# Kernel tuning notes

Measured on AMD Instinct MI355X. Metric: run time of the kernel, lower is better.

Reference implementation:

```python
import jax, jax.numpy as jnp
import numpy as np

DIM = 2048
N_HEADS = 16
HEAD_DIM = DIM // N_HEADS

def setup_inputs() -> dict:
    key = jax.random.key(0)
    kx, kqkv, kout = jax.random.split(key, 3)
    x = jax.random.normal(kx, (2, 2048, DIM), dtype=jnp.float32)
    # nn.Linear weights stored [out_features, in_features]; y = x @ W.T
    W_qkv = jax.random.normal(kqkv, (3 * DIM, DIM), dtype=jnp.float32) * (DIM ** -0.5)
    W_out = jax.random.normal(kout, (DIM, DIM), dtype=jnp.float32) * (DIM ** -0.5)
    return {"x": x, "W_qkv": W_qkv, "W_out": W_out}

def reference(x, W_qkv, W_out):
    B, T, D = x.shape
    qkv = jnp.einsum('btd,ed->bte', x, W_qkv)  # [B,T,3D]
    q, k, v = jnp.split(qkv, 3, axis=-1)
    def heads(t):
        return t.reshape(B, T, N_HEADS, HEAD_DIM).transpose(0, 2, 1, 3)  # [B,H,T,d]
    q, k, v = heads(q), heads(k), heads(v)
    att = jnp.einsum('bhid,bhjd->bhij', q, k) / (HEAD_DIM ** 0.5)
    causal = jnp.tril(jnp.ones((T, T), dtype=bool))
    att = jnp.where(causal, att, -jnp.inf)
    att = jax.nn.softmax(att, axis=-1)
    out = jnp.einsum('bhij,bhjd->bhid', att, v)
    out = out.transpose(0, 2, 1, 3).reshape(B, T, D)
    return jnp.einsum('btd,ed->bte', out, W_out)
```

## Files before the change

### kernel.cpp

```cpp
#include <hip/hip_runtime.h>

typedef short short8 __attribute__((ext_vector_type(8)));
typedef short short4v __attribute__((ext_vector_type(4)));
typedef float f32x4 __attribute__((ext_vector_type(4)));
typedef unsigned short u16;
typedef u16 ushort4v __attribute__((ext_vector_type(4)));

__device__ inline u16 f2bf(float f){
  unsigned int u = __builtin_bit_cast(unsigned int, f);
  u = (u + 0x7fffu + ((u >> 16) & 1u)) >> 16;
  return (u16)u;
}

__device__ inline short8 cat8(short4v a, short4v b){
  short8 r;
  r[0]=a[0]; r[1]=a[1]; r[2]=a[2]; r[3]=a[3];
  r[4]=b[0]; r[5]=b[1]; r[6]=b[2]; r[7]=b[3];
  return r;
}

__device__ inline void gload_lds16(const void* g, unsigned lds_addr){
  __builtin_amdgcn_global_load_lds((__attribute__((address_space(1))) void*)(uintptr_t)g,
                                   (__attribute__((address_space(3))) void*)(uintptr_t)lds_addr,
                                   16, 0, 0);
}

__global__ void cvt_bf16(const float* __restrict__ in, u16* __restrict__ out, int n4){
  int stride = gridDim.x * blockDim.x;
  for (int i = blockIdx.x * blockDim.x + threadIdx.x; i < n4; i += stride){
    float4 v = ((const float4*)in)[i];
    ushort4v r = { f2bf(v.x), f2bf(v.y), f2bf(v.z), f2bf(v.w) };
    ((ushort4v*)out)[i] = r;
  }
}

#define BARRIER() { __builtin_amdgcn_sched_barrier(0); __builtin_amdgcn_s_barrier(); __builtin_amdgcn_sched_barrier(0); }
#define VM4() asm volatile("s_waitcnt vmcnt(4)" ::: "memory");

#define MFMA4(MO, AA, BB) { __builtin_amdgcn_s_setprio(1); \
  _Pragma("unroll") for (int m = 0; m < 4; m++) \
    _Pragma("unroll") for (int n = 0; n < 4; n++) \
      acc[(MO)+m][n] = __builtin_amdgcn_mfma_f32_16x16x32_bf16(AA[(MO)+m], BB[n], acc[(MO)+m][n], 0, 0, 0); \
  __builtin_amdgcn_s_setprio(0); }

#define PHASE4(ABASE, BBASE, ST1, ST2, ST3, ST4) { \
    const u16* Ab = (ABASE); const u16* Bb = (BBASE); \
    short8 a0[8], b0[4], a1[8], b1[4]; \
    _Pragma("unroll") for (int m = 0; m < 8; m++){ int row = wm*128 + m*16 + lr; int ph = lg ^ (row & 7); a0[m] = *(const short8*)&Ab[row*64 + ph*8]; } \
    _Pragma("unroll") for (int n = 0; n < 4; n++){ int row = wn*64 + n*16 + lr; int ph = lg ^ (row & 7); b0[n] = *(const short8*)&Bb[row*64 + ph*8]; } \
    ST1 BARRIER() MFMA4(0, a0, b0) BARRIER() \
    _Pragma("unroll") for (int m = 0; m < 8; m++){ int row = wm*128 + m*16 + lr; int ph = (4+lg) ^ (row & 7); a1[m] = *(const short8*)&Ab[row*64 + ph*8]; } \
    _Pragma("unroll") for (int n = 0; n < 4; n++){ int row = wn*64 + n*16 + lr; int ph = (4+lg) ^ (row & 7); b1[n] = *(const short8*)&Bb[row*64 + ph*8]; } \
    ST2 BARRIER() MFMA4(4, a0, b0) BARRIER() \
    ST3 BARRIER() MFMA4(0, a1, b1) BARRIER() \
    ST4 VM4() BARRIER() MFMA4(4, a1, b1) BARRIER() \
  }

template<int OUT_BF16>
__global__ __launch_bounds__(512, 2) void gemm256(const u16* __restrict__ A, const u16* __restrict__ B,
                                                  void* __restrict__ Cv, int M, int N, int K){
  __shared__ u16 lds[2][32768];
  const int tid = threadIdx.x, wave = tid >> 6, lane = tid & 63;
  const int lr = lane & 15, lg = lane >> 4;
  const int wm = wave >> 2, wn = wave & 3;
  const long bm = blockIdx.x * 256L, bn = blockIdx.y * 256L;
  const int l3 = lane >> 3, l7 = lane & 7;

  const u16* asrc = A + (bm + wave*8 + l3) * (long)K + (l7 ^ l3) * 8;
  const u16* bsrc = B + (bn + wave*8 + l3) * (long)K + (l7 ^ l3) * 8;
  const unsigned ldsbase = (unsigned)(uintptr_t)&lds[0][0];
  const unsigned wdst = wave * 1024u;

#define STG_A(BUF,S,KOFF) gload_lds16(asrc + (size_t)(S)*64*K + (KOFF), ldsbase + (BUF)*65536u + wdst + (S)*8192u);
#define STG_B(BUF,S,KOFF) gload_lds16(bsrc + (size_t)(S)*64*K + (KOFF), ldsbase + (BUF)*65536u + 32768u + wdst + (S)*8192u);

  f32x4 acc[8][4] = {};
  const int nk = K >> 6;

  #pragma unroll
  for (int s = 0; s < 4; s++){ STG_A(0, s, 0) }
  #pragma unroll
  for (int s = 0; s < 4; s++){ STG_B(0, s, 0) }
  #pragma unroll
  for (int s = 0; s < 4; s++){ STG_A(1, s, 64) }
  VM4()
  BARRIER()

  for (int i = 0; i < (nk >> 1); i++){
    const size_t kt1 = (size_t)((2*i + 1) << 6);
    const size_t kn0 = (size_t)(((2*i + 2) & (nk - 1)) << 6);
    const size_t kn1 = (size_t)(((2*i + 3) & (nk - 1)) << 6);
    PHASE4(&lds[0][0], &lds[0][16384],
           STG_B(1,0,kt1) STG_B(1,1,kt1),
           STG_B(1,2,kt1) STG_B(1,3,kt1),
           STG_A(0,0,kn0) STG_A(0,1,kn0),
           STG_A(0,2,kn0) STG_A(0,3,kn0))
    PHASE4(&lds[1][0], &lds[1][16384],
           STG_B(0,0,kn0) STG_B(0,1,kn0),
           STG_B(0,2,kn0) STG_B(0,3,kn0),
           STG_A(1,0,kn1) STG_A(1,1,kn1),
           STG_A(1,2,kn1) STG_A(1,3,kn1))
  }
#undef STG_A
#undef STG_B

  #pragma unroll
  for (int m = 0; m < 8; m++){
    #pragma unroll
    for (int n = 0; n < 4; n++){
      #pragma unroll
      for (int r = 0; r < 4; r++){
        long row = bm + wm*128 + m*16 + lg*4 + r;
        long col = bn + wn*64 + n*16 + lr;
        float v = acc[m][n][r];
        if (OUT_BF16) ((u16*)Cv)[row * (long)N + col] = f2bf(v);
        else          ((float*)Cv)[row * (long)N + col] = v;
      }
    }
  }
}

template<int OUT_BF16>
__global__ __launch_bounds__(512, 2) void gemm_bt2(const u16* __restrict__ A, const u16* __restrict__ B,
                                                   void* __restrict__ Cv, int M, int N, int K){
  __shared__ u16 lds[2][24576];
  const int tid = threadIdx.x, wave = tid >> 6, lane = tid & 63;
  const int lr = lane & 15, lg = lane >> 4;
  const int wm = wave >> 2, wn = wave & 3;
  const long bm = blockIdx.x * 128L, bn = blockIdx.y * 256L;
  const int l3 = lane >> 3, l7 = lane & 7;

  const u16* asrc = A + (bm + wave * 8 + l3) * (long)K + (l7 ^ l3) * 8;
  const u16* bsrc = B + (bn + wave * 8 + l3) * (long)K + (l7 ^ l3) * 8;
  const unsigned ldsbase = (unsigned)(uintptr_t)&lds[0][0];
  const unsigned adst = wave * 1024u;
  const unsigned bdst = 16384u + wave * 1024u;

  #define STAGE(BUF, K0) { \
    unsigned bb = ldsbase + (unsigned)(BUF) * 49152u; \
    gload_lds16(asrc + (K0),                       bb + adst); \
    gload_lds16(asrc + 64 * (size_t)K + (K0),      bb + adst + 8192u); \
    gload_lds16(bsrc + (K0),                       bb + bdst); \
    gload_lds16(bsrc + 64 * (size_t)K + (K0),      bb + bdst + 8192u); \
    gload_lds16(bsrc + 128 * (size_t)K + (K0),     bb + bdst + 16384u); \
    gload_lds16(bsrc + 192 * (size_t)K + (K0),     bb + bdst + 24576u); \
  }

  f32x4 acc[4][4] = {};
  const int nk = K >> 6;
  int cur = 0;

  STAGE(0, 0)
  asm volatile("s_waitcnt vmcnt(0)" ::: "memory");
  BARRIER()

  for (int t = 0; t < nk; ++t){
    if (t + 1 < nk){
      STAGE(cur ^ 1, (t + 1) * 64)
      asm volatile("s_waitcnt vmcnt(6)" ::: "memory");
    } else {
      asm volatile("s_waitcnt vmcnt(0)" ::: "memory");
    }
    BARRIER()

    const u16* Ab = &lds[cur][0];
    const u16* Bb = &lds[cur][8192];
    short8 af[2][4], bfr[2][4];
    #pragma unroll
    for (int kk = 0; kk < 2; kk++){
      #pragma unroll
      for (int m = 0; m < 4; m++){
        int row = wm * 64 + m * 16 + lr;
        int phys = (kk * 4 + lg) ^ (row & 7);
        af[kk][m] = *(const short8*)&Ab[row * 64 + phys * 8];
      }
      #pragma unroll
      for (int n = 0; n < 4; n++){
        int row = wn * 64 + n * 16 + lr;
        int phys = (kk * 4 + lg) ^ (row & 7);
        bfr[kk][n] = *(const short8*)&Bb[row * 64 + phys * 8];
      }
    }
    __builtin_amdgcn_s_setprio(1);
    #pragma unroll
    for (int m = 0; m < 4; m++)
      #pragma unroll
      for (int n = 0; n < 4; n++){
        acc[m][n] = __builtin_amdgcn_mfma_f32_16x16x32_bf16(af[0][m], bfr[0][n], acc[m][n], 0, 0, 0);
        acc[m][n] = __builtin_amdgcn_mfma_f32_16x16x32_bf16(af[1][m], bfr[1][n], acc[m][n], 0, 0, 0);
      }
    __builtin_amdgcn_s_setprio(0);
    BARRIER()
    cur ^= 1;
  }
  #undef STAGE

  #pragma unroll
  for (int m = 0; m < 4; m++){
    #pragma unroll
    for (int n = 0; n < 4; n++){
      #pragma unroll
      for (int r = 0; r < 4; r++){
        long row = bm + wm*64 + m*16 + lg*4 + r;
        long col = bn + wn*64 + n*16 + lr;
        float v = acc[m][n][r];
        if (OUT_BF16) ((u16*)Cv)[row * (long)N + col] = f2bf(v);
        else          ((float*)Cv)[row * (long)N + col] = v;
      }
    }
  }
}

__global__ __launch_bounds__(512, 2) void attn_fwd(const u16* __restrict__ qkv, u16* __restrict__ out){
  const int T = 2048, D3 = 6144, D = 2048, HD = 128;
  const int bh = blockIdx.x;
  const int pr = blockIdx.y;
  const int b = bh >> 4, h = bh & 15;
  const int tid = threadIdx.x, wave = tid >> 6, lane = tid & 63;
  const int lr = lane & 15, lg = lane >> 4;

  __shared__ u16 Klds[64][136];
  __shared__ u16 Vlds[64][136];
  __shared__ u16 Plds[8][16][72];

  const size_t base = (size_t)b * T * D3;
  const unsigned vtr = (unsigned)(uintptr_t)&Vlds[(lane >> 4) * 8 + ((lane >> 2) & 3)][(lane & 3) * 4];

  const int srow = tid >> 4;
  const int scol = (tid & 15) * 8;
  const u16* kgp = qkv + base + (size_t)srow * D3 + D + h * HD + scol;
  const u16* vgp = kgp + D;

  for (int half = 0; half < 2; half++){
    const int qt = half ? pr : (15 - pr);
    const int q0 = qt * 128;
    const int q0w = q0 + wave * 16;

    short8 qf[4];
    {
      const u16* qrow = qkv + base + (size_t)(q0w + lr) * D3 + h * HD;
      #pragma unroll
      for (int kk = 0; kk < 4; kk++)
        qf[kk] = *(const short8*)(qrow + kk*32 + lg*8);
    }

    f32x4 o[8] = {};
    float mrow[4], lrw[4];
    #pragma unroll
    for (int r = 0; r < 4; r++){ mrow[r] = -1e30f; lrw[r] = 0.f; }

    const int ntiles = (q0 + 128) >> 6;
    short8 kreg[2], vreg[2];
    #pragma unroll
    for (int c = 0; c < 2; c++){
      kreg[c] = *(const short8*)(kgp + (size_t)(32 * c) * D3);
      vreg[c] = *(const short8*)(vgp + (size_t)(32 * c) * D3);
    }

    for (int t = 0; t < ntiles; t++){
      const int k0 = t * 64;
      __syncthreads();
      #pragma unroll
      for (int c = 0; c < 2; c++){
        *(short8*)&Klds[srow + 32*c][scol] = kreg[c];
        *(short8*)&Vlds[srow + 32*c][scol] = vreg[c];
      }
      __syncthreads();
      if (t + 1 < ntiles){
        const u16* kn = kgp + (size_t)(k0 + 64) * D3;
        const u16* vn = vgp + (size_t)(k0 + 64) * D3;
        #pragma unroll
        for (int c = 0; c < 2; c++){
          kreg[c] = *(const short8*)(kn + (size_t)(32 * c) * D3);
          vreg[c] = *(const short8*)(vn + (size_t)(32 * c) * D3);
        }
      }

      if (k0 <= q0w + 15){
        f32x4 s[4] = {};
        #pragma unroll
        for (int kh = 0; kh < 4; kh++){
          #pragma unroll
          for (int kk = 0; kk < 4; kk++){
            short8 kfrag = *(const short8*)&Klds[kh*16 + lr][kk*32 + lg*8];
            s[kh] = __builtin_amdgcn_mfma_f32_16x16x32_bf16(qf[kk], kfrag, s[kh], 0, 0, 0);
          }
        }
        const float scale = 0.08838834764831845f;
        const bool need_mask = (k0 + 63 > q0w);
        #pragma unroll
        for (int kh = 0; kh < 4; kh++){
          int key = k0 + kh*16 + lr;
          #pragma unroll
          for (int r = 0; r < 4; r++){
            float v = s[kh][r] * scale;
            if (need_mask && key > q0w + lg*4 + r) v = -1e30f;
            s[kh][r] = v;
          }
        }
        float fs[4];
        #pragma unroll
        for (int r = 0; r < 4; r++){
          float mx = fmaxf(fmaxf(s[0][r], s[1][r]), fmaxf(s[2][r], s[3][r]));
          #pragma unroll
          for (int msk = 8; msk >= 1; msk >>= 1)
            mx = fmaxf(mx, __shfl_xor(mx, msk, 64));
          float mnew = fmaxf(mrow[r], mx);
          float f = __expf(mrow[r] - mnew);
          float p0 = __expf(s[0][r] - mnew);
          float p1 = __expf(s[1][r] - mnew);
          float p2 = __expf(s[2][r] - mnew);
          float p3 = __expf(s[3][r] - mnew);
          s[0][r] = p0; s[1][r] = p1; s[2][r] = p2; s[3][r] = p3;
          float rs = (p0 + p1) + (p2 + p3);
          #pragma unroll
          for (int msk = 8; msk >= 1; msk >>= 1)
            rs += __shfl_xor(rs, msk, 64);
          lrw[r] = lrw[r] * f + rs;
          mrow[r] = mnew;
          fs[r] = f;
        }
        #pragma unroll
        for (int dt = 0; dt < 8; dt++)
          #pragma unroll
          for (int r = 0; r < 4; r++)
            o[dt][r] *= fs[r];
        #pragma unroll
        for (int kh = 0; kh < 4; kh++)
          #pragma unroll
          for (int r = 0; r < 4; r++)
            Plds[wave][lg*4 + r][kh*16 + lr] = f2bf(s[kh][r]);
        asm volatile("s_waitcnt lgkmcnt(0)" ::: "memory");
        __builtin_amdgcn_sched_barrier(0);
        short8 pf[2];
        #pragma unroll
        for (int kp2 = 0; kp2 < 2; kp2++)
          pf[kp2] = *(const short8*)&Plds[wave][lr][kp2*32 + lg*8];
        asm volatile("s_waitcnt lgkmcnt(0)" ::: "memory");
        __builtin_amdgcn_sched_barrier(0);

        short4v vf[2][2][2];
        #define TR4(BUF, PTR) \
          asm volatile("ds_read_b64_tr_b16 %0, %1"             : "=v"(vf[BUF][0][0]) : "v"(PTR)); \
          asm volatile("ds_read_b64_tr_b16 %0, %1 offset:1088" : "=v"(vf[BUF][0][1]) : "v"(PTR)); \
          asm volatile("ds_read_b64_tr_b16 %0, %1 offset:8704" : "=v"(vf[BUF][1][0]) : "v"(PTR)); \
          asm volatile("ds_read_b64_tr_b16 %0, %1 offset:9792" : "=v"(vf[BUF][1][1]) : "v"(PTR));
        TR4(0, vtr)
        #pragma unroll
        for (int dt = 0; dt < 8; dt++){
          if (dt < 7){
            unsigned pn = vtr + (unsigned)((dt + 1) * 32);
            TR4((dt + 1) & 1, pn)
            asm volatile("s_waitcnt lgkmcnt(4)" ::: "memory");
          } else {
            asm volatile("s_waitcnt lgkmcnt(0)" ::: "memory");
          }
          __builtin_amdgcn_sched_barrier(0);
          short8 v0 = cat8(vf[dt & 1][0][0], vf[dt & 1][0][1]);
          short8 v1 = cat8(vf[dt & 1][1][0], vf[dt & 1][1][1]);
          o[dt] = __builtin_amdgcn_mfma_f32_16x16x32_bf16(pf[0], v0, o[dt], 0, 0, 0);
          o[dt] = __builtin_amdgcn_mfma_f32_16x16x32_bf16(pf[1], v1, o[dt], 0, 0, 0);
        }
        #undef TR4
      }
    }
    float rl[4];
    #pragma unroll
    for (int r = 0; r < 4; r++) rl[r] = 1.0f / lrw[r];
    #pragma unroll
    for (int dt = 0; dt < 8; dt++){
      #pragma unroll
      for (int r = 0; r < 4; r++){
        float v = o[dt][r] * rl[r];
        int qa = q0w + lg*4 + r;
        out[(size_t)(b * T + qa) * D + h * HD + dt*16 + lr] = f2bf(v);
      }
    }
  }
}

extern "C" void kernel_launch(void* const* d_in, const int* in_sizes, int n_in,
                              void* d_out, int out_size, void* d_ws, size_t ws_size,
                              hipStream_t stream) {
  const float* x    = (const float*)d_in[0];
  const float* wqkv = (const float*)d_in[1];
  const float* wout = (const float*)d_in[2];
  float* out = (float*)d_out;

  u16* ws    = (u16*)d_ws;
  u16* xb    = ws;
  u16* wqkvb = xb + 8388608;
  u16* qkvb  = wqkvb + 12582912;
  u16* attnb = xb;
  u16* woutb = wqkvb;

  cvt_bf16<<<2048, 256, 0, stream>>>(x,    xb,    8388608 / 4);
  cvt_bf16<<<2048, 256, 0, stream>>>(wqkv, wqkvb, 12582912 / 4);

  gemm256<1><<<dim3(16, 24), 512, 0, stream>>>(xb, wqkvb, qkvb, 4096, 6144, 2048);

  cvt_bf16<<<2048, 256, 0, stream>>>(wout, woutb, 4194304 / 4);

  attn_fwd<<<dim3(32, 8), 512, 0, stream>>>(qkvb, attnb);

  gemm_bt2<0><<<dim3(32, 8), 512, 0, stream>>>(attnb, woutb, out, 4096, 2048, 2048);
}
```

Measured before the change: 266.3 us.

## Split QKV GEMM, replace out-proj GEMM, add lazy softmax rescaling

The QKV projection is split into two launches: the 256x256 kernel covers the Q/K columns and a new simpler single-buffered 128x128 gemm_bt covers the V columns. The output projection also moves from the double-buffered 128x256 kernel to that 128x128 kernel with 256 threads and synchronous LDS staging. Attention folds log2(e) into the scale so it can use exp2f. It also skips the running-max update and the output rescale when every row's new max stays within a threshold of the old one. These aim to improve tile scheduling on the GEMMs and cut exp and rescale work in attention, at the cost of losing load/compute overlap in the simpler GEMM and accepting larger intermediate exponents.

```diff
diff --git a/kernel.cpp b/kernel.cpp
--- a/kernel.cpp
+++ b/kernel.cpp
@@ -58,7 +58,7 @@
 
 template<int OUT_BF16>
 __global__ __launch_bounds__(512, 2) void gemm256(const u16* __restrict__ A, const u16* __restrict__ B,
-                                                  void* __restrict__ Cv, int M, int N, int K){
+                                                  void* __restrict__ Cv, int M, int NS, int K){
   __shared__ u16 lds[2][32768];
   const int tid = threadIdx.x, wave = tid >> 6, lane = tid & 63;
   const int lr = lane & 15, lg = lane >> 4;
@@ -113,88 +113,63 @@
         long row = bm + wm*128 + m*16 + lg*4 + r;
         long col = bn + wn*64 + n*16 + lr;
         float v = acc[m][n][r];
-        if (OUT_BF16) ((u16*)Cv)[row * (long)N + col] = f2bf(v);
-        else          ((float*)Cv)[row * (long)N + col] = v;
+        if (OUT_BF16) ((u16*)Cv)[row * (long)NS + col] = f2bf(v);
+        else          ((float*)Cv)[row * (long)NS + col] = v;
       }
     }
   }
 }
 
 template<int OUT_BF16>
-__global__ __launch_bounds__(512, 2) void gemm_bt2(const u16* __restrict__ A, const u16* __restrict__ B,
-                                                   void* __restrict__ Cv, int M, int N, int K){
-  __shared__ u16 lds[2][24576];
-  const int tid = threadIdx.x, wave = tid >> 6, lane = tid & 63;
+__global__ __launch_bounds__(256) void gemm_bt(const u16* __restrict__ A, const u16* __restrict__ B,
+                                               void* __restrict__ Cv, int M, int NS, int K){
+  __shared__ u16 As[128 * 64];
+  __shared__ u16 Bs[128 * 64];
+  const int tid  = threadIdx.x;
+  const int wave = tid >> 6, lane = tid & 63;
   const int lr = lane & 15, lg = lane >> 4;
-  const int wm = wave >> 2, wn = wave & 3;
-  const long bm = blockIdx.x * 128L, bn = blockIdx.y * 256L;
-  const int l3 = lane >> 3, l7 = lane & 7;
-
-  const u16* asrc = A + (bm + wave * 8 + l3) * (long)K + (l7 ^ l3) * 8;
-  const u16* bsrc = B + (bn + wave * 8 + l3) * (long)K + (l7 ^ l3) * 8;
-  const unsigned ldsbase = (unsigned)(uintptr_t)&lds[0][0];
-  const unsigned adst = wave * 1024u;
-  const unsigned bdst = 16384u + wave * 1024u;
-
-  #define STAGE(BUF, K0) { \
-    unsigned bb = ldsbase + (unsigned)(BUF) * 49152u; \
-    gload_lds16(asrc + (K0),                       bb + adst); \
-    gload_lds16(asrc + 64 * (size_t)K + (K0),      bb + adst + 8192u); \
-    gload_lds16(bsrc + (K0),                       bb + bdst); \
-    gload_lds16(bsrc + 64 * (size_t)K + (K0),      bb + bdst + 8192u); \
-    gload_lds16(bsrc + 128 * (size_t)K + (K0),     bb + bdst + 16384u); \
-    gload_lds16(bsrc + 192 * (size_t)K + (K0),     bb + bdst + 24576u); \
-  }
+  const int wm = wave >> 1, wn = wave & 1;
+  const long bm = blockIdx.x * 128L, bn = blockIdx.y * 128L;
+  const unsigned asb = (unsigned)(uintptr_t)As;
+  const unsigned bsb = (unsigned)(uintptr_t)Bs;
+
+  const int  srow = wave * 32 + (lane >> 3);
+  const int  scol = ((lane & 7) ^ (lane >> 3)) * 8;
+  const u16* aptr = A + (bm + srow) * (long)K + scol;
+  const u16* bptr = B + (bn + srow) * (long)K + scol;
+  const unsigned sdst = (unsigned)(wave * 4096);
 
   f32x4 acc[4][4] = {};
-  const int nk = K >> 6;
-  int cur = 0;
-
-  STAGE(0, 0)
-  asm volatile("s_waitcnt vmcnt(0)" ::: "memory");
-  BARRIER()
-
-  for (int t = 0; t < nk; ++t){
-    if (t + 1 < nk){
-      STAGE(cur ^ 1, (t + 1) * 64)
-      asm volatile("s_waitcnt vmcnt(6)" ::: "memory");
-    } else {
-      asm volatile("s_waitcnt vmcnt(0)" ::: "memory");
-    }
-    BARRIER()
-
-    const u16* Ab = &lds[cur][0];
-    const u16* Bb = &lds[cur][8192];
-    short8 af[2][4], bfr[2][4];
+  for (int k0 = 0; k0 < K; k0 += 64){
+    #pragma unroll
+    for (int c = 0; c < 4; c++){
+      gload_lds16(aptr + (size_t)(8 * c) * K + k0, asb + sdst + 1024u * c);
+      gload_lds16(bptr + (size_t)(8 * c) * K + k0, bsb + sdst + 1024u * c);
+    }
+    __syncthreads();
     #pragma unroll
     for (int kk = 0; kk < 2; kk++){
+      short8 af[4], bfr[4];
       #pragma unroll
       for (int m = 0; m < 4; m++){
         int row = wm * 64 + m * 16 + lr;
         int phys = (kk * 4 + lg) ^ (row & 7);
-        af[kk][m] = *(const short8*)&Ab[row * 64 + phys * 8];
+        af[m] = *(const short8*)&As[row * 64 + phys * 8];
       }
       #pragma unroll
       for (int n = 0; n < 4; n++){
         int row = wn * 64 + n * 16 + lr;
         int phys = (kk * 4 + lg) ^ (row & 7);
-        bfr[kk][n] = *(const short8*)&Bb[row * 64 + phys * 8];
-      }
-    }
-    __builtin_amdgcn_s_setprio(1);
-    #pragma unroll
-    for (int m = 0; m < 4; m++)
-      #pragma unroll
-      for (int n = 0; n < 4; n++){
-        acc[m][n] = __builtin_amdgcn_mfma_f32_16x16x32_bf16(af[0][m], bfr[0][n], acc[m][n], 0, 0, 0);
-        acc[m][n] = __builtin_amdgcn_mfma_f32_16x16x32_bf16(af[1][m], bfr[1][n], acc[m][n], 0, 0, 0);
-      }
-    __builtin_amdgcn_s_setprio(0);
-    BARRIER()
-    cur ^= 1;
-  }
-  #undef STAGE
-
+        bfr[n] = *(const short8*)&Bs[row * 64 + phys * 8];
+      }
+      #pragma unroll
+      for (int m = 0; m < 4; m++)
+        #pragma unroll
+        for (int n = 0; n < 4; n++)
+          acc[m][n] = __builtin_amdgcn_mfma_f32_16x16x32_bf16(af[m], bfr[n], acc[m][n], 0, 0, 0);
+    }
+    __syncthreads();
+  }
   #pragma unroll
   for (int m = 0; m < 4; m++){
     #pragma unroll
@@ -204,8 +179,8 @@
         long row = bm + wm*64 + m*16 + lg*4 + r;
         long col = bn + wn*64 + n*16 + lr;
         float v = acc[m][n][r];
-        if (OUT_BF16) ((u16*)Cv)[row * (long)N + col] = f2bf(v);
-        else          ((float*)Cv)[row * (long)N + col] = v;
+        if (OUT_BF16) ((u16*)Cv)[row * (long)NS + col] = f2bf(v);
+        else          ((float*)Cv)[row * (long)NS + col] = v;
       }
     }
   }
@@ -231,6 +206,9 @@
   const u16* kgp = qkv + base + (size_t)srow * D3 + D + h * HD + scol;
   const u16* vgp = kgp + D;
 
+  const float scale2 = 0.12751971252971732f;
+  const float THR = 11.5f;
+
   for (int half = 0; half < 2; half++){
     const int qt = half ? pr : (15 - pr);
     const int q0 = qt * 128;
@@ -286,45 +264,67 @@
             s[kh] = __builtin_amdgcn_mfma_f32_16x16x32_bf16(qf[kk], kfrag, s[kh], 0, 0, 0);
           }
         }
-        const float scale = 0.08838834764831845f;
         const bool need_mask = (k0 + 63 > q0w);
         #pragma unroll
         for (int kh = 0; kh < 4; kh++){
           int key = k0 + kh*16 + lr;
           #pragma unroll
           for (int r = 0; r < 4; r++){
-            float v = s[kh][r] * scale;
+            float v = s[kh][r] * scale2;
             if (need_mask && key > q0w + lg*4 + r) v = -1e30f;
             s[kh][r] = v;
           }
         }
-        float fs[4];
+        float mx[4];
         #pragma unroll
         for (int r = 0; r < 4; r++){
-          float mx = fmaxf(fmaxf(s[0][r], s[1][r]), fmaxf(s[2][r], s[3][r]));
+          float m0 = fmaxf(fmaxf(s[0][r], s[1][r]), fmaxf(s[2][r], s[3][r]));
           #pragma unroll
           for (int msk = 8; msk >= 1; msk >>= 1)
-            mx = fmaxf(mx, __shfl_xor(mx, msk, 64));
-          float mnew = fmaxf(mrow[r], mx);
-          float f = __expf(mrow[r] - mnew);
-          float p0 = __expf(s[0][r] - mnew);
-          float p1 = __expf(s[1][r] - mnew);
-          float p2 = __expf(s[2][r] - mnew);
-          float p3 = __expf(s[3][r] - mnew);
-          s[0][r] = p0; s[1][r] = p1; s[2][r] = p2; s[3][r] = p3;
-          float rs = (p0 + p1) + (p2 + p3);
-          #pragma unroll
-          for (int msk = 8; msk >= 1; msk >>= 1)
-            rs += __shfl_xor(rs, msk, 64);
-          lrw[r] = lrw[r] * f + rs;
-          mrow[r] = mnew;
-          fs[r] = f;
-        }
-        #pragma unroll
-        for (int dt = 0; dt < 8; dt++)
-          #pragma unroll
-          for (int r = 0; r < 4; r++)
-            o[dt][r] *= fs[r];
+            m0 = fmaxf(m0, __shfl_xor(m0, msk, 64));
+          mx[r] = m0;
+        }
+        bool cnd = (mx[0] <= mrow[0] + THR) && (mx[1] <= mrow[1] + THR) &&
+                   (mx[2] <= mrow[2] + THR) && (mx[3] <= mrow[3] + THR);
+        if (__all(cnd)){
+          #pragma unroll
+          for (int r = 0; r < 4; r++){
+            float p0 = exp2f(s[0][r] - mrow[r]);
+            float p1 = exp2f(s[1][r] - mrow[r]);
+            float p2 = exp2f(s[2][r] - mrow[r]);
+            float p3 = exp2f(s[3][r] - mrow[r]);
+            s[0][r] = p0; s[1][r] = p1; s[2][r] = p2; s[3][r] = p3;
+            float rs = (p0 + p1) + (p2 + p3);
+            #pragma unroll
+            for (int msk = 8; msk >= 1; msk >>= 1)
+              rs += __shfl_xor(rs, msk, 64);
+            lrw[r] += rs;
+          }
+        } else {
+          float fs[4];
+          #pragma unroll
+          for (int r = 0; r < 4; r++){
+            float mnew = fmaxf(mrow[r], mx[r]);
+            float f = exp2f(mrow[r] - mnew);
+            float p0 = exp2f(s[0][r] - mnew);
+            float p1 = exp2f(s[1][r] - mnew);
+            float p2 = exp2f(s[2][r] - mnew);
+            float p3 = exp2f(s[3][r] - mnew);
+            s[0][r] = p0; s[1][r] = p1; s[2][r] = p2; s[3][r] = p3;
+            float rs = (p0 + p1) + (p2 + p3);
+            #pragma unroll
+            for (int msk = 8; msk >= 1; msk >>= 1)
+              rs += __shfl_xor(rs, msk, 64);
+            lrw[r] = lrw[r] * f + rs;
+            mrow[r] = mnew;
+            fs[r] = f;
+          }
+          #pragma unroll
+          for (int dt = 0; dt < 8; dt++)
+            #pragma unroll
+            for (int r = 0; r < 4; r++)
+              o[dt][r] *= fs[r];
+        }
         #pragma unroll
         for (int kh = 0; kh < 4; kh++)
           #pragma unroll
@@ -397,11 +397,13 @@
   cvt_bf16<<<2048, 256, 0, stream>>>(x,    xb,    8388608 / 4);
   cvt_bf16<<<2048, 256, 0, stream>>>(wqkv, wqkvb, 12582912 / 4);
 
-  gemm256<1><<<dim3(16, 24), 512, 0, stream>>>(xb, wqkvb, qkvb, 4096, 6144, 2048);
+  gemm256<1><<<dim3(16, 16), 512, 0, stream>>>(xb, wqkvb, qkvb, 4096, 6144, 2048);
+  gemm_bt<1><<<dim3(32, 16), 256, 0, stream>>>(xb, wqkvb + (size_t)4096 * 2048,
+                                               qkvb + 4096, 4096, 6144, 2048);
 
   cvt_bf16<<<2048, 256, 0, stream>>>(wout, woutb, 4194304 / 4);
 
   attn_fwd<<<dim3(32, 8), 512, 0, stream>>>(qkvb, attnb);
 
-  gemm_bt2<0><<<dim3(32, 8), 512, 0, stream>>>(attnb, woutb, out, 4096, 2048, 2048);
-}
+  gemm_bt<0><<<dim3(32, 16), 256, 0, stream>>>(attnb, woutb, out, 4096, 2048, 2048);
+}
```

After: 268.0 us. Within noise of the previous version (+0.6%).
